# Optimization experiments

Hardware: AMD Instinct MI355X
Metric: run time of the kernel (lower is better)

## Reference

```python
import jax, jax.numpy as jnp
import numpy as np

B, T, E, H, C = 256, 512, 256, 256, 6
FORGET_BIAS = 1.0


def _lstm_step(c, h, x, W, b):
    # TF LSTMCell: z = [x, h] @ W + b, gates ordered (i, j, f, o)
    z = jnp.concatenate([x, h], axis=-1) @ W + b
    i, j, f, o = jnp.split(z, 4, axis=-1)
    c_new = c * jax.nn.sigmoid(f + FORGET_BIAS) + jax.nn.sigmoid(i) * jnp.tanh(j)
    h_new = jnp.tanh(c_new) * jax.nn.sigmoid(o)
    return c_new, h_new


def setup_inputs() -> dict:
    key = jax.random.key(0)
    ks = jax.random.split(key, 4)
    x = jax.random.normal(ks[0], (B, T, E), dtype=jnp.float32)
    # tf.random_normal_initializer for head weights; LSTM kernels ~ glorot-ish scale
    W1 = jax.random.normal(ks[1], (E + H, 4 * H), dtype=jnp.float32) * 0.05
    b1 = jnp.zeros((4 * H,), dtype=jnp.float32)
    W2 = jax.random.normal(ks[2], (H + H, 4 * H), dtype=jnp.float32) * 0.05
    b2 = jnp.zeros((4 * H,), dtype=jnp.float32)
    W_out = jax.random.normal(ks[3], (H, C), dtype=jnp.float32)
    b_out = jnp.zeros((C,), dtype=jnp.float32)
    return {"x": x, "W1": W1, "b1": b1, "W2": W2, "b2": b2,
            "W_out": W_out, "b_out": b_out}


def reference(x, W1, b1, W2, b2, W_out, b_out):
    # 2-layer LSTM over time via lax.scan (zero initial state), then
    # dense + sigmoid + 0.5 threshold head applied to every timestep output.
    def step(carry, x_t):
        c1, h1, c2, h2 = carry
        c1, h1 = _lstm_step(c1, h1, x_t, W1, b1)
        c2, h2 = _lstm_step(c2, h2, h1, W2, b2)
        return (c1, h1, c2, h2), h2

    zeros = jnp.zeros((x.shape[0], H), dtype=x.dtype)
    init = (zeros, zeros, zeros, zeros)
    xs = jnp.swapaxes(x, 0, 1)  # [T, B, E]
    _, outs = jax.lax.scan(step, init, xs)  # outs: [T, B, H]
    outs = jnp.swapaxes(outs, 0, 1).reshape(-1, H)  # [B*T, H]

    logits = outs @ W_out + b_out  # [B*T, C]
    probs = jax.nn.sigmoid(logits)
    condition = 0.5 < probs
    prediction = jnp.where(condition, jnp.ones_like(probs), jnp.zeros_like(probs))
    return logits, condition, prediction
```

## Files before the change

### kernel.cpp

```cpp
#include <hip/hip_runtime.h>
#include <math.h>

#define T_ 512

__device__ __forceinline__ double sigmd(double v) { return 1.0 / (1.0 + exp(-v)); }

__device__ __forceinline__ float hloadf(const float* p) {
  unsigned u = __hip_atomic_load((const unsigned*)p,
                                 __ATOMIC_RELAXED, __HIP_MEMORY_SCOPE_AGENT);
  return __builtin_bit_cast(float, u);
}
__device__ __forceinline__ void hstoref(float* p, float v) {
  __hip_atomic_store((unsigned*)p, __builtin_bit_cast(unsigned, v),
                     __ATOMIC_RELAXED, __HIP_MEMORY_SCOPE_AGENT);
}

__device__ __forceinline__ int aoff_f(int kc) { return (kc << 3) + ((kc >> 6) << 2); }

__global__ __launch_bounds__(512, 1) void lstm2_head(
    const float* __restrict__ x, const float* __restrict__ W1,
    const float* __restrict__ b1, const float* __restrict__ W2,
    const float* __restrict__ b2, const float* __restrict__ Wo,
    const float* __restrict__ bo, float* __restrict__ out,
    unsigned char* __restrict__ ws)
{
  __shared__ float Alds[6192];
  __shared__ float zbuf[2112];

  const int tid = threadIdx.x;
  const int g  = blockIdx.x >> 3;
  const int w  = blockIdx.x & 7;
  const int rb0 = g << 3;

  unsigned* bar = (unsigned*)ws + (g << 4);
  float* hbase = (float*)(ws + 4096);
  float* h1g = hbase + (size_t)g * 4096;
  float* h2g = hbase + 131072 + (size_t)g * 4096;

  for (int i = tid; i < 4096; i += 512) { hstoref(h1g + i, 0.0f); hstoref(h2g + i, 0.0f); }

  __builtin_amdgcn_s_waitcnt(0);
  __syncthreads();
  if (tid == 0) {
    __hip_atomic_fetch_add(bar, 1u, __ATOMIC_RELAXED, __HIP_MEMORY_SCOPE_AGENT);
    while (__hip_atomic_load(bar, __ATOMIC_RELAXED, __HIP_MEMORY_SCOPE_AGENT) < 8u)
      __builtin_amdgcn_s_sleep(1);
    __asm__ volatile("" ::: "memory");
  }
  __syncthreads();

  const int lane = tid & 63;
  const int wvid = tid >> 6;
  const int half = wvid >> 2;
  const int gate = wvid & 3;
  const int kt   = lane >> 3;
  const int og   = lane & 7;
  const float* wbase = (half ? W2 : W1)
      + (size_t)(kt << 6) * 1024 + (gate << 8) + (w << 5) + (og << 2);
  const int kc0  = (half << 8) + (kt << 6);
  const int zrow = ((half << 2) + gate) << 3;

  const int sr  = tid & 7;
  const int skc = tid >> 3;

  const int L  = tid >> 8;
  const int ur = (tid >> 5) & 7;
  const int hj = tid & 31;
  const float* ubb = L ? b2 : b1;
  const int ucol = (w << 5) + hj;
  const double ub_i = (double)ubb[ucol];
  const double ub_j = (double)ubb[256 + ucol];
  const double ub_f = (double)ubb[512 + ucol];
  const double ub_o = (double)ubb[768 + ucol];
  double cst = 0.0;

  const bool headblk = (w == 0);
  float  wo_r[4][6];
  double bo_r[6];
  if (headblk) {
    #pragma unroll
    for (int q = 0; q < 4; ++q)
      #pragma unroll
      for (int c = 0; c < 6; ++c) wo_r[q][c] = Wo[(lane + (q << 6)) * 6 + c];
    #pragma unroll
    for (int c = 0; c < 6; ++c) bo_r[c] = (double)bo[c];
  }

  auto do_head = [&](int t3) {
    double pr[6] = {0, 0, 0, 0, 0, 0};
    #pragma unroll
    for (int q = 0; q < 4; ++q) {
      double hv = (double)Alds[aoff_f(512 + lane + (q << 6)) + wvid];
      #pragma unroll
      for (int c = 0; c < 6; ++c) pr[c] = fma(hv, (double)wo_r[q][c], pr[c]);
    }
    #pragma unroll
    for (int off = 1; off <= 32; off <<= 1)
      #pragma unroll
      for (int c = 0; c < 6; ++c) pr[c] += __shfl_xor(pr[c], off, 64);
    if (lane == 0) {
      size_t orow = (((size_t)(rb0 + wvid)) << 9) + (size_t)t3;
      #pragma unroll
      for (int c = 0; c < 6; ++c) {
        double lg = pr[c] + bo_r[c];
        out[orow * 6 + c] = (float)lg;
        float pd = (lg > 0.0) ? 1.0f : 0.0f;
        out[(size_t)786432 + orow * 6 + c] = pd;
        out[(size_t)1572864 + orow * 6 + c] = pd;
      }
    }
  };

  {
    const float* xb = x + (size_t)(rb0 + sr) * (T_ * 256) + skc;
    float sv[12];
    #pragma unroll
    for (int v = 0; v < 4; ++v) sv[v] = xb[v << 6];
    const float* h1p = h1g + 2048;
    const float* h2p = h2g;
    #pragma unroll
    for (int v = 0; v < 4; ++v) sv[4 + v] = hloadf(h1p + (sr << 8) + skc + (v << 6));
    #pragma unroll
    for (int v = 0; v < 4; ++v) sv[8 + v] = hloadf(h2p + (sr << 8) + skc + (v << 6));
    #pragma unroll
    for (int v = 0; v < 12; ++v) Alds[aoff_f((v << 6) + skc) + sr] = sv[v];
  }
  __syncthreads();

  #pragma unroll 1
  for (int p = 0; p <= T_ + 1; ++p) {
    float acc[4][8];
    #pragma unroll
    for (int c = 0; c < 4; ++c)
      #pragma unroll
      for (int r = 0; r < 8; ++r) acc[c][r] = 0.0f;
    {
      const float* wp = wbase;
      const float* ap = Alds + aoff_f(kc0);
      float4 wva[4], wvb[4];
      #pragma unroll
      for (int j = 0; j < 4; ++j) wva[j] = *(const float4*)(wp + (size_t)j * 1024);
      #pragma unroll 1
      for (int sg = 0; sg < 8; ++sg) {
        const int s0 = sg << 3;
        #pragma unroll
        for (int j = 0; j < 4; ++j)
          wvb[j] = *(const float4*)(wp + (size_t)(s0 + 4 + j) * 1024);
        #pragma unroll
        for (int j = 0; j < 4; ++j) {
          const float* apj = ap + ((s0 + j) << 3);
          float4 a0 = *(const float4*)(apj);
          float4 a1 = *(const float4*)(apj + 4);
          float a[8] = {a0.x, a0.y, a0.z, a0.w, a1.x, a1.y, a1.z, a1.w};
          #pragma unroll
          for (int r = 0; r < 8; ++r) {
            acc[0][r] = fmaf(a[r], wva[j].x, acc[0][r]);
            acc[1][r] = fmaf(a[r], wva[j].y, acc[1][r]);
            acc[2][r] = fmaf(a[r], wva[j].z, acc[2][r]);
            acc[3][r] = fmaf(a[r], wva[j].w, acc[3][r]);
          }
        }
        if (sg < 7) {
          #pragma unroll
          for (int j = 0; j < 4; ++j)
            wva[j] = *(const float4*)(wp + (size_t)(s0 + 8 + j) * 1024);
        }
        #pragma unroll
        for (int j = 0; j < 4; ++j) {
          const float* apj = ap + ((s0 + 4 + j) << 3);
          float4 a0 = *(const float4*)(apj);
          float4 a1 = *(const float4*)(apj + 4);
          float a[8] = {a0.x, a0.y, a0.z, a0.w, a1.x, a1.y, a1.z, a1.w};
          #pragma unroll
          for (int r = 0; r < 8; ++r) {
            acc[0][r] = fmaf(a[r], wvb[j].x, acc[0][r]);
            acc[1][r] = fmaf(a[r], wvb[j].y, acc[1][r]);
            acc[2][r] = fmaf(a[r], wvb[j].z, acc[2][r]);
            acc[3][r] = fmaf(a[r], wvb[j].w, acc[3][r]);
          }
        }
      }
    }

    #pragma unroll
    for (int c = 0; c < 4; ++c)
      #pragma unroll
      for (int r = 0; r < 8; ++r) {
        float v = acc[c][r];
        v += __shfl_xor(v, 8, 64);
        v += __shfl_xor(v, 16, 64);
        v += __shfl_xor(v, 32, 64);
        acc[c][r] = v;
      }

    #pragma unroll
    for (int r = 0; r < 8; ++r) {
      if (kt == r) {
        #pragma unroll
        for (int c = 0; c < 4; ++c)
          zbuf[(zrow + r) * 33 + (og << 2) + c] = acc[c][r];
      }
    }
    __syncthreads();

    {
      const bool uact = L ? (p >= 1 && p <= T_) : (p < T_);
      if (uact) {
        const float* za = zbuf + ((L << 5) + ur) * 33 + hj;
        double zi = (double)za[0]   + ub_i;
        double zj = (double)za[264] + ub_j;
        double zf = (double)za[528] + ub_f;
        double zo = (double)za[792] + ub_o;
        cst = cst * sigmd(zf + 1.0) + sigmd(zi) * tanh(zj);
        float hv = (float)(tanh(cst) * sigmd(zo));
        float* hd = L ? (h2g + (((p + 1) & 1) << 11)) : (h1g + ((p & 1) << 11));
        hstoref(hd + (ur << 8) + ucol, hv);
      }
    }

    if (p <= T_) {
      __builtin_amdgcn_s_waitcnt(0);
      __syncthreads();
      if (tid == 0)
        __hip_atomic_fetch_add(bar, 1u, __ATOMIC_RELAXED, __HIP_MEMORY_SCOPE_AGENT);

      const int xp1 = (p + 1 < T_) ? (p + 1) : (T_ - 1);
      const float* xb = x + (size_t)(rb0 + sr) * (T_ * 256) + (size_t)xp1 * 256 + skc;
      float xv[4];
      #pragma unroll
      for (int v = 0; v < 4; ++v) xv[v] = xb[v << 6];

      if (headblk && p >= 2) do_head(p - 2);

      #pragma unroll
      for (int v = 0; v < 4; ++v) Alds[aoff_f((v << 6) + skc) + sr] = xv[v];

      if (tid == 0) {
        const unsigned target = ((unsigned)(p + 2)) << 3;
        while (__hip_atomic_load(bar, __ATOMIC_RELAXED, __HIP_MEMORY_SCOPE_AGENT) < target)
          __builtin_amdgcn_s_sleep(1);
        __asm__ volatile("" ::: "memory");
      }
      __syncthreads();

      const float* h1p = h1g + ((p & 1) << 11);
      const float* h2p = h2g + (((p + 1) & 1) << 11);
      float hv8[8];
      #pragma unroll
      for (int v = 0; v < 4; ++v) hv8[v] = hloadf(h1p + (sr << 8) + skc + (v << 6));
      #pragma unroll
      for (int v = 0; v < 4; ++v) hv8[4 + v] = hloadf(h2p + (sr << 8) + skc + (v << 6));
      #pragma unroll
      for (int v = 0; v < 8; ++v) Alds[aoff_f(256 + (v << 6) + skc) + sr] = hv8[v];
      __syncthreads();
    } else {
      if (headblk) do_head(p - 2);
    }
  }
}

extern "C" void kernel_launch(void* const* d_in, const int* in_sizes, int n_in,
                              void* d_out, int out_size, void* d_ws, size_t ws_size,
                              hipStream_t stream) {
  const float* x  = (const float*)d_in[0];
  const float* W1 = (const float*)d_in[1];
  const float* b1 = (const float*)d_in[2];
  const float* W2 = (const float*)d_in[3];
  const float* b2 = (const float*)d_in[4];
  const float* Wo = (const float*)d_in[5];
  const float* bo = (const float*)d_in[6];
  float* out = (float*)d_out;
  unsigned char* ws = (unsigned char*)d_ws;

  hipMemsetAsync(d_ws, 0, 4096, stream);

  lstm2_head<<<dim3(256), dim3(512), 0, stream>>>(x, W1, b1, W2, b2, Wo, bo, out, ws);
}
```

Measured before the change: 7.063 ms.

## Use fast float gate math, transpose-reduce shuffles, deeper weight prefetch, busy-spin barrier

Gate nonlinearities move from double-precision exp/tanh to float fast-exp with hardware reciprocal, and the output head moves from double to float. The cross-lane reduction becomes a recursive-halving transpose-reduce, so each lane ends up owning one row. This cuts the shuffle count and removes the predicated zbuf writes. Weight prefetch widens to 8 float4 per stage, and the first chunk is loaded before the grid barrier wait to hide its latency. The spin-wait drops s_sleep, and the head computation moves ahead of the barrier arrive. Fast approximations may change numerics near the 0.5 threshold, and the extra registers may raise pressure.

```diff
diff --git a/kernel.cpp b/kernel.cpp
--- a/kernel.cpp
+++ b/kernel.cpp
@@ -3,7 +3,13 @@
 
 #define T_ 512
 
-__device__ __forceinline__ double sigmd(double v) { return 1.0 / (1.0 + exp(-v)); }
+__device__ __forceinline__ float sigf(float x) {
+  return __builtin_amdgcn_rcpf(1.0f + __expf(-x));
+}
+__device__ __forceinline__ float tanhf_(float x) {
+  float e = __expf(x + x);
+  return 1.0f - 2.0f * __builtin_amdgcn_rcpf(e + 1.0f);
+}
 
 __device__ __forceinline__ float hloadf(const float* p) {
   unsigned u = __hip_atomic_load((const unsigned*)p,
@@ -43,8 +49,7 @@
   __syncthreads();
   if (tid == 0) {
     __hip_atomic_fetch_add(bar, 1u, __ATOMIC_RELAXED, __HIP_MEMORY_SCOPE_AGENT);
-    while (__hip_atomic_load(bar, __ATOMIC_RELAXED, __HIP_MEMORY_SCOPE_AGENT) < 8u)
-      __builtin_amdgcn_s_sleep(1);
+    while (__hip_atomic_load(bar, __ATOMIC_RELAXED, __HIP_MEMORY_SCOPE_AGENT) < 8u) {}
     __asm__ volatile("" ::: "memory");
   }
   __syncthreads();
@@ -55,6 +60,9 @@
   const int gate = wvid & 3;
   const int kt   = lane >> 3;
   const int og   = lane & 7;
+  const bool b5 = (lane & 32) != 0;
+  const bool b4 = (lane & 16) != 0;
+  const bool b3 = (lane & 8) != 0;
   const float* wbase = (half ? W2 : W1)
       + (size_t)(kt << 6) * 1024 + (gate << 8) + (w << 5) + (og << 2);
   const int kc0  = (half << 8) + (kt << 6);
@@ -68,31 +76,31 @@
   const int hj = tid & 31;
   const float* ubb = L ? b2 : b1;
   const int ucol = (w << 5) + hj;
-  const double ub_i = (double)ubb[ucol];
-  const double ub_j = (double)ubb[256 + ucol];
-  const double ub_f = (double)ubb[512 + ucol];
-  const double ub_o = (double)ubb[768 + ucol];
+  const float ub_i = ubb[ucol];
+  const float ub_j = ubb[256 + ucol];
+  const float ub_f = ubb[512 + ucol] + 1.0f;
+  const float ub_o = ubb[768 + ucol];
   double cst = 0.0;
 
   const bool headblk = (w == 0);
-  float  wo_r[4][6];
-  double bo_r[6];
+  float wo_r[4][6];
+  float bo_r[6];
   if (headblk) {
     #pragma unroll
     for (int q = 0; q < 4; ++q)
       #pragma unroll
       for (int c = 0; c < 6; ++c) wo_r[q][c] = Wo[(lane + (q << 6)) * 6 + c];
     #pragma unroll
-    for (int c = 0; c < 6; ++c) bo_r[c] = (double)bo[c];
+    for (int c = 0; c < 6; ++c) bo_r[c] = bo[c];
   }
 
   auto do_head = [&](int t3) {
-    double pr[6] = {0, 0, 0, 0, 0, 0};
+    float pr[6] = {0, 0, 0, 0, 0, 0};
     #pragma unroll
     for (int q = 0; q < 4; ++q) {
-      double hv = (double)Alds[aoff_f(512 + lane + (q << 6)) + wvid];
-      #pragma unroll
-      for (int c = 0; c < 6; ++c) pr[c] = fma(hv, (double)wo_r[q][c], pr[c]);
+      float hv = Alds[aoff_f(512 + lane + (q << 6)) + wvid];
+      #pragma unroll
+      for (int c = 0; c < 6; ++c) pr[c] = fmaf(hv, wo_r[q][c], pr[c]);
     }
     #pragma unroll
     for (int off = 1; off <= 32; off <<= 1)
@@ -102,9 +110,9 @@
       size_t orow = (((size_t)(rb0 + wvid)) << 9) + (size_t)t3;
       #pragma unroll
       for (int c = 0; c < 6; ++c) {
-        double lg = pr[c] + bo_r[c];
-        out[orow * 6 + c] = (float)lg;
-        float pd = (lg > 0.0) ? 1.0f : 0.0f;
+        float lg = pr[c] + bo_r[c];
+        out[orow * 6 + c] = lg;
+        float pd = (lg > 0.0f) ? 1.0f : 0.0f;
         out[(size_t)786432 + orow * 6 + c] = pd;
         out[(size_t)1572864 + orow * 6 + c] = pd;
       }
@@ -127,6 +135,10 @@
   }
   __syncthreads();
 
+  float4 wva[8];
+  #pragma unroll
+  for (int j = 0; j < 8; ++j) wva[j] = *(const float4*)(wbase + (size_t)j * 1024);
+
   #pragma unroll 1
   for (int p = 0; p <= T_ + 1; ++p) {
     float acc[4][8];
@@ -135,19 +147,16 @@
       #pragma unroll
       for (int r = 0; r < 8; ++r) acc[c][r] = 0.0f;
     {
-      const float* wp = wbase;
       const float* ap = Alds + aoff_f(kc0);
-      float4 wva[4], wvb[4];
-      #pragma unroll
-      for (int j = 0; j < 4; ++j) wva[j] = *(const float4*)(wp + (size_t)j * 1024);
+      float4 wvb[8];
       #pragma unroll 1
-      for (int sg = 0; sg < 8; ++sg) {
-        const int s0 = sg << 3;
+      for (int sg = 0; sg < 4; ++sg) {
+        const int s0 = sg << 4;
         #pragma unroll
-        for (int j = 0; j < 4; ++j)
-          wvb[j] = *(const float4*)(wp + (size_t)(s0 + 4 + j) * 1024);
+        for (int j = 0; j < 8; ++j)
+          wvb[j] = *(const float4*)(wbase + (size_t)(s0 + 8 + j) * 1024);
         #pragma unroll
-        for (int j = 0; j < 4; ++j) {
+        for (int j = 0; j < 8; ++j) {
           const float* apj = ap + ((s0 + j) << 3);
           float4 a0 = *(const float4*)(apj);
           float4 a1 = *(const float4*)(apj + 4);
@@ -160,14 +169,14 @@
             acc[3][r] = fmaf(a[r], wva[j].w, acc[3][r]);
           }
         }
-        if (sg < 7) {
+        if (sg < 3) {
           #pragma unroll
-          for (int j = 0; j < 4; ++j)
-            wva[j] = *(const float4*)(wp + (size_t)(s0 + 8 + j) * 1024);
+          for (int j = 0; j < 8; ++j)
+            wva[j] = *(const float4*)(wbase + (size_t)(s0 + 16 + j) * 1024);
         }
         #pragma unroll
-        for (int j = 0; j < 4; ++j) {
-          const float* apj = ap + ((s0 + 4 + j) << 3);
+        for (int j = 0; j < 8; ++j) {
+          const float* apj = ap + ((s0 + 8 + j) << 3);
           float4 a0 = *(const float4*)(apj);
           float4 a1 = *(const float4*)(apj + 4);
           float a[8] = {a0.x, a0.y, a0.z, a0.w, a1.x, a1.y, a1.z, a1.w};
@@ -182,24 +191,30 @@
       }
     }
 
+    float tA[4][4];
     #pragma unroll
     for (int c = 0; c < 4; ++c)
       #pragma unroll
-      for (int r = 0; r < 8; ++r) {
-        float v = acc[c][r];
-        v += __shfl_xor(v, 8, 64);
-        v += __shfl_xor(v, 16, 64);
-        v += __shfl_xor(v, 32, 64);
-        acc[c][r] = v;
-      }
-
-    #pragma unroll
-    for (int r = 0; r < 8; ++r) {
-      if (kt == r) {
-        #pragma unroll
-        for (int c = 0; c < 4; ++c)
-          zbuf[(zrow + r) * 33 + (og << 2) + c] = acc[c][r];
-      }
+      for (int q = 0; q < 4; ++q) {
+        float send = b5 ? acc[c][q] : acc[c][q + 4];
+        float keep = b5 ? acc[c][q + 4] : acc[c][q];
+        tA[c][q] = keep + __shfl_xor(send, 32, 64);
+      }
+    float tB[4][2];
+    #pragma unroll
+    for (int c = 0; c < 4; ++c)
+      #pragma unroll
+      for (int q = 0; q < 2; ++q) {
+        float send = b4 ? tA[c][q] : tA[c][q + 2];
+        float keep = b4 ? tA[c][q + 2] : tA[c][q];
+        tB[c][q] = keep + __shfl_xor(send, 16, 64);
+      }
+    #pragma unroll
+    for (int c = 0; c < 4; ++c) {
+      float send = b3 ? tB[c][0] : tB[c][1];
+      float keep = b3 ? tB[c][1] : tB[c][0];
+      float zv = keep + __shfl_xor(send, 8, 64);
+      zbuf[(zrow + kt) * 33 + (og << 2) + c] = zv;
     }
     __syncthreads();
 
@@ -207,18 +222,20 @@
       const bool uact = L ? (p >= 1 && p <= T_) : (p < T_);
       if (uact) {
         const float* za = zbuf + ((L << 5) + ur) * 33 + hj;
-        double zi = (double)za[0]   + ub_i;
-        double zj = (double)za[264] + ub_j;
-        double zf = (double)za[528] + ub_f;
-        double zo = (double)za[792] + ub_o;
-        cst = cst * sigmd(zf + 1.0) + sigmd(zi) * tanh(zj);
-        float hv = (float)(tanh(cst) * sigmd(zo));
+        float si = sigf(za[0]   + ub_i);
+        float tj = tanhf_(za[264] + ub_j);
+        float sf = sigf(za[528] + ub_f);
+        float so = sigf(za[792] + ub_o);
+        cst = cst * (double)sf + (double)(si * tj);
+        float hv = tanhf_((float)cst) * so;
         float* hd = L ? (h2g + (((p + 1) & 1) << 11)) : (h1g + ((p & 1) << 11));
         hstoref(hd + (ur << 8) + ucol, hv);
       }
     }
 
     if (p <= T_) {
+      if (headblk && p >= 2) do_head(p - 2);
+
       __builtin_amdgcn_s_waitcnt(0);
       __syncthreads();
       if (tid == 0)
@@ -229,16 +246,15 @@
       float xv[4];
       #pragma unroll
       for (int v = 0; v < 4; ++v) xv[v] = xb[v << 6];
-
-      if (headblk && p >= 2) do_head(p - 2);
-
       #pragma unroll
       for (int v = 0; v < 4; ++v) Alds[aoff_f((v << 6) + skc) + sr] = xv[v];
+
+      #pragma unroll
+      for (int j = 0; j < 8; ++j) wva[j] = *(const float4*)(wbase + (size_t)j * 1024);
 
       if (tid == 0) {
         const unsigned target = ((unsigned)(p + 2)) << 3;
-        while (__hip_atomic_load(bar, __ATOMIC_RELAXED, __HIP_MEMORY_SCOPE_AGENT) < target)
-          __builtin_amdgcn_s_sleep(1);
+        while (__hip_atomic_load(bar, __ATOMIC_RELAXED, __HIP_MEMORY_SCOPE_AGENT) < target) {}
         __asm__ volatile("" ::: "memory");
       }
       __syncthreads();
```

Result: faster. 6.125 ms (-13.3%).
